# Performance work log

Measured on AMD Instinct MI355X. Metric: run time of the kernel, lower is better.

## Reference

```python
import jax, jax.numpy as jnp
import numpy as np

D_MODEL = 1024
NUM_HEADS = 16
DEPTH = D_MODEL // NUM_HEADS


def setup_inputs() -> dict:
    key = jax.random.key(0)
    ks = jax.random.split(key, 11)
    B, S, D = 2, 2048, D_MODEL
    s = 1.0 / np.sqrt(D)
    inp = {
        'x': jax.random.normal(ks[0], (B, S, D), jnp.float32),
        'pH': jax.random.normal(ks[1], (B, 1, 1), jnp.float32),
        'Wq': jax.random.normal(ks[2], (D, D), jnp.float32) * s,
        'bq': jnp.zeros((D,), jnp.float32),
        'Wk': jax.random.normal(ks[3], (D, D), jnp.float32) * s,
        'bk': jnp.zeros((D,), jnp.float32),
        'Wv': jax.random.normal(ks[4], (D, D), jnp.float32) * s,
        'bv': jnp.zeros((D,), jnp.float32),
        'Wo': jax.random.normal(ks[5], (D, D), jnp.float32) * s,
        'bo': jnp.zeros((D,), jnp.float32),
    }
    return inp


def reference(x, pH, Wq, bq, Wk, bk, Wv, bv, Wo, bo):
    B, S, D = x.shape
    H, dh = NUM_HEADS, DEPTH
    # QKV projections -> [B, H, S, dh]
    def proj(W, b):
        return (x @ W + b).reshape(B, S, H, dh).transpose(0, 2, 1, 3)
    q = proj(Wq, bq)
    k = proj(Wk, bk)
    v = proj(Wv, bv)
    # scores [B, H, S, S] with additive per-sample pH bias broadcast over heads/positions
    scores = jnp.einsum('bhqd,bhkd->bhqk', q, k) / jnp.sqrt(jnp.asarray(dh, x.dtype))
    scores = scores + pH[:, :, :, None]  # [B,1,1,1] broadcasts to [B,H,S,S]
    attn = jax.nn.softmax(scores, axis=-1)
    out = jnp.einsum('bhqk,bhkd->bhqd', attn, v)  # [B,H,S,dh]
    out = out.transpose(0, 2, 1, 3).reshape(B, S, D)
    return out @ Wo + bo  # dropout p=0.0 -> identity
```

## Files before the change

### kernel.cpp

```cpp
#include <hip/hip_runtime.h>
#include <hip/hip_bf16.h>
#include <math.h>

#define BATCH 2
#define SEQ   2048
#define DMODEL 1024
#define NHEADS 16
#define DHEAD 64
#define MROWS (BATCH*SEQ)

typedef __attribute__((ext_vector_type(8))) short bf16x8;
typedef __attribute__((ext_vector_type(4))) short bf16x4;
typedef __attribute__((ext_vector_type(4))) float f32x4;

__device__ __forceinline__ short f2bf(float f) {
    union { float f; unsigned u; } c; c.f = f;
    unsigned r = (c.u + 0x7fffu + ((c.u >> 16) & 1u)) >> 16;
    return (short)r;
}
__device__ __forceinline__ float bf2f(short h) {
    union { unsigned u; float f; } c; c.u = ((unsigned)(unsigned short)h) << 16;
    return c.f;
}

__device__ __forceinline__ void async_ld16(const void* g, void* l) {
    __builtin_amdgcn_global_load_lds(
        (const __attribute__((address_space(1))) unsigned*)g,
        (__attribute__((address_space(3))) unsigned*)l, 16, 0, 0);
}

__device__ __forceinline__ void pl32swap(unsigned &a, unsigned &b) {
    asm("v_permlane32_swap_b32 %0, %1" : "+v"(a), "+v"(b));
}
__device__ __forceinline__ void pl16swap(unsigned &a, unsigned &b) {
    asm("v_permlane16_swap_b32 %0, %1" : "+v"(a), "+v"(b));
}
__device__ __forceinline__ bf16x8 mk8(unsigned a, unsigned b, unsigned c, unsigned d) {
    union { unsigned u[4]; bf16x8 h; } t;
    t.u[0] = a; t.u[1] = b; t.u[2] = c; t.u[3] = d; return t.h;
}

__global__ __launch_bounds__(256) void prep(
    const float* __restrict__ x, short* __restrict__ xhi,
    const float* __restrict__ W0, const float* __restrict__ W1,
    const float* __restrict__ W2, const float* __restrict__ W3,
    short* __restrict__ oqkv, short* __restrict__ oo)
{
    __shared__ float T[64][65];
    const int tid = threadIdx.x;
    if (blockIdx.x < 2048) {
        const int i = blockIdx.x * 256 + tid;
        const float4* p = (const float4*)x + (size_t)i * 2;
        float4 a = p[0], b = p[1];
        float v[8] = {a.x, a.y, a.z, a.w, b.x, b.y, b.z, b.w};
        bf16x8 H;
        #pragma unroll
        for (int j = 0; j < 8; ++j) H[j] = f2bf(v[j]);
        *((bf16x8*)xhi + i) = H;
        return;
    }
    const int bi = blockIdx.x - 2048;
    const int z = bi >> 8;
    const int t = bi & 255;
    const float* W = (z == 0) ? W0 : (z == 1) ? W1 : (z == 2) ? W2 : W3;
    short* out = (z < 3) ? (oqkv + (size_t)z * 1024 * 1024) : oo;
    const int n0 = (t & 15) * 64, k0 = (t >> 4) * 64;
    #pragma unroll
    for (int i = 0; i < 16; ++i) {
        const int idx = tid + i * 256;
        const int r = idx >> 6, c = idx & 63;
        T[r][c] = W[(size_t)(k0 + r) * DMODEL + n0 + c];
    }
    __syncthreads();
    #pragma unroll
    for (int i = 0; i < 4; ++i) {
        const int idx = tid + i * 256;
        const int r = idx >> 4, g = idx & 15;
        bf16x4 H;
        #pragma unroll
        for (int j = 0; j < 4; ++j)
            H[j] = f2bf(T[g * 4 + j][r]);
        *(bf16x4*)(out + (size_t)(n0 + r) * DMODEL + k0 + g * 4) = H;
    }
}

__global__ __launch_bounds__(256, 3) void qkv_gemm(
    const short* __restrict__ Ahi, const short* __restrict__ Bthi,
    const float* __restrict__ b0, const float* __restrict__ b1, const float* __restrict__ b2,
    short* __restrict__ oqh, short* __restrict__ okh, short* __restrict__ ovh,
    float qscale)
{
    __shared__ short Ah[128 * 64], Bh[128 * 64];

    const int tid  = threadIdx.x;
    const int lane = tid & 63;
    const int w    = tid >> 6;
    const int quad = lane >> 4;
    const int l15  = lane & 15;
    const int wr   = w >> 1, wc = w & 1;
    const int m0   = blockIdx.y * 128;
    const int n0   = blockIdx.x * 128;
    const int K    = DMODEL;

    f32x4 acc[4][4] = {};

    for (int k0 = 0; k0 < K; k0 += 64) {
        __syncthreads();
        #pragma unroll
        for (int j = 0; j < 8; ++j) {
            const int base = w * 512 + j * 64;
            const int c = base + lane;
            if (base < 1024) {
                const int row = c >> 3, pos = (c & 7) ^ (row & 7);
                async_ld16(Ahi + (size_t)(m0 + row) * K + k0 + pos * 8, Ah + base * 8);
            } else {
                const int cb = c - 1024;
                const int row = cb >> 3, pos = (cb & 7) ^ (row & 7);
                async_ld16(Bthi + (size_t)(n0 + row) * K + k0 + pos * 8, Bh + (base - 1024) * 8);
            }
        }
        __syncthreads();

        #pragma unroll
        for (int s = 0; s < 2; ++s) {
            bf16x8 afh[4], bfh[4];
            #pragma unroll
            for (int mi = 0; mi < 4; ++mi) {
                const int row = wr * 64 + mi * 16 + l15;
                const int pos = (s * 4 + quad) ^ (row & 7);
                afh[mi] = *(const bf16x8*)(Ah + row * 64 + pos * 8);
            }
            #pragma unroll
            for (int ni = 0; ni < 4; ++ni) {
                const int row = wc * 64 + ni * 16 + l15;
                const int pos = (s * 4 + quad) ^ (row & 7);
                bfh[ni] = *(const bf16x8*)(Bh + row * 64 + pos * 8);
            }
            #pragma unroll
            for (int mi = 0; mi < 4; ++mi)
                #pragma unroll
                for (int ni = 0; ni < 4; ++ni)
                    acc[mi][ni] = __builtin_amdgcn_mfma_f32_16x16x32_bf16(
                        afh[mi], bfh[ni], acc[mi][ni], 0, 0, 0);
        }
    }

    const int nbase = n0 + wc * 64;
    const int which = nbase >> 10;
    const int hh = (nbase & 1023) >> 6;
    const int mb = m0 + wr * 64;
    const int b = mb >> 11, sbase = mb & (SEQ - 1);
    __syncthreads();
    short* scr = (w < 2) ? (Ah + w * 4096) : (Bh + (w - 2) * 4096);

    if (which < 2) {
        const float* bias = which ? b1 : b0;
        short* dstp = which ? okh : oqh;
        const float scl = which ? 1.0f : qscale;
        #pragma unroll
        for (int mi = 0; mi < 4; ++mi)
            #pragma unroll
            for (int ni = 0; ni < 4; ++ni)
                #pragma unroll
                for (int r = 0; r < 4; ++r) {
                    const int sloc = mi * 16 + quad * 4 + r;
                    const int dloc = ni * 16 + l15;
                    const int nn = (nbase + ni * 16 + l15) & 1023;
                    scr[sloc * 64 + (((dloc >> 3) ^ (sloc & 7)) * 8) + (dloc & 7)] =
                        f2bf((acc[mi][ni][r] + bias[nn]) * scl);
                }
        #pragma unroll
        for (int i = 0; i < 8; ++i) {
            const int sloc = i * 8 + (lane >> 3);
            const int cph = (lane & 7) ^ (sloc & 7);
            bf16x8 row = *(const bf16x8*)(scr + sloc * 64 + cph * 8);
            const int dloc = (lane & 7) * 8;
            *(bf16x8*)(dstp + ((size_t)(b * NHEADS + hh) * SEQ + sbase + sloc) * DHEAD + dloc) = row;
        }
    } else {
        #pragma unroll
        for (int mi = 0; mi < 4; ++mi)
            #pragma unroll
            for (int ni = 0; ni < 4; ++ni)
                #pragma unroll
                for (int r = 0; r < 4; ++r) {
                    const int sloc = mi * 16 + quad * 4 + r;
                    const int dloc = ni * 16 + l15;
                    const int nn = (nbase + ni * 16 + l15) & 1023;
                    scr[dloc * 64 + (((sloc >> 3) ^ (dloc & 7)) * 8) + (sloc & 7)] =
                        f2bf(acc[mi][ni][r] + b2[nn]);
                }
        #pragma unroll
        for (int i = 0; i < 8; ++i) {
            const int dloc = i * 8 + (lane >> 3);
            const int cph = (lane & 7) ^ (dloc & 7);
            bf16x8 row = *(const bf16x8*)(scr + dloc * 64 + cph * 8);
            const int sg = sbase + (lane & 7) * 8;
            *(bf16x8*)(ovh + ((size_t)(b * NHEADS + hh) * DHEAD + dloc) * SEQ + sg) = row;
        }
    }
}

__global__ __launch_bounds__(256) void ogemm(
    const short* __restrict__ Ahi, const short* __restrict__ Bthi,
    const float* __restrict__ b0, float* __restrict__ outf)
{
    __shared__ short Ah[64 * 64], Bh[128 * 64];

    const int tid  = threadIdx.x;
    const int lane = tid & 63;
    const int w    = tid >> 6;
    const int quad = lane >> 4;
    const int l15  = lane & 15;
    const int wr   = w >> 1, wc = w & 1;
    const int m0   = blockIdx.y * 64;
    const int n0   = blockIdx.x * 128;
    const int K    = DMODEL;

    f32x4 acc[2][4] = {};

    for (int k0 = 0; k0 < K; k0 += 64) {
        __syncthreads();
        #pragma unroll
        for (int j = 0; j < 6; ++j) {
            const int base = w * 384 + j * 64;
            const int c = base + lane;
            if (base < 512) {
                const int row = c >> 3, pos = (c & 7) ^ (row & 7);
                async_ld16(Ahi + (size_t)(m0 + row) * K + k0 + pos * 8, Ah + base * 8);
            } else {
                const int cb = c - 512;
                const int row = cb >> 3, pos = (cb & 7) ^ (row & 7);
                async_ld16(Bthi + (size_t)(n0 + row) * K + k0 + pos * 8, Bh + (base - 512) * 8);
            }
        }
        __syncthreads();

        #pragma unroll
        for (int s = 0; s < 2; ++s) {
            bf16x8 afh[2], bfh[4];
            #pragma unroll
            for (int mi = 0; mi < 2; ++mi) {
                const int row = wr * 32 + mi * 16 + l15;
                const int pos = (s * 4 + quad) ^ (row & 7);
                afh[mi] = *(const bf16x8*)(Ah + row * 64 + pos * 8);
            }
            #pragma unroll
            for (int ni = 0; ni < 4; ++ni) {
                const int row = wc * 64 + ni * 16 + l15;
                const int pos = (s * 4 + quad) ^ (row & 7);
                bfh[ni] = *(const bf16x8*)(Bh + row * 64 + pos * 8);
            }
            #pragma unroll
            for (int mi = 0; mi < 2; ++mi)
                #pragma unroll
                for (int ni = 0; ni < 4; ++ni)
                    acc[mi][ni] = __builtin_amdgcn_mfma_f32_16x16x32_bf16(
                        afh[mi], bfh[ni], acc[mi][ni], 0, 0, 0);
        }
    }

    #pragma unroll
    for (int mi = 0; mi < 2; ++mi)
        #pragma unroll
        for (int ni = 0; ni < 4; ++ni)
            #pragma unroll
            for (int r = 0; r < 4; ++r) {
                const int m = m0 + wr * 32 + mi * 16 + quad * 4 + r;
                const int nn = n0 + wc * 64 + ni * 16 + l15;
                outf[(size_t)m * DMODEL + nn] = acc[mi][ni][r] + b0[nn];
            }
}

__global__ __launch_bounds__(256) void attn_mfma(
    const short* __restrict__ Qh_g, const short* __restrict__ Kh_g,
    const short* __restrict__ Vth_g,
    short* __restrict__ op0, float* __restrict__ l0g)
{
    __shared__ short Ksh[4096];
    __shared__ short Vsh[4096];

    const int tid  = threadIdx.x;
    const int lane = tid & 63;
    const int w    = tid >> 6;
    const int quad = lane >> 4;
    const int l15  = lane & 15;

    const int bh    = blockIdx.x & 31;
    const int sk    = (blockIdx.x >> 5) & 3;
    const int qtile = blockIdx.x >> 7;
    const int q0    = qtile * 128 + w * 32;
    const size_t kvb = (size_t)bh * SEQ * DHEAD;

    bf16x8 ones;
    #pragma unroll
    for (int j = 0; j < 8; ++j) ones[j] = (short)0x3f80;

    bf16x8 qA[2], qB[2];
    {
        const size_t qrA = kvb + (size_t)(q0 + l15) * DHEAD;
        const size_t qrB = kvb + (size_t)(q0 + 16 + l15) * DHEAD;
        qA[0] = *(const bf16x8*)(Qh_g + qrA + quad * 8);
        qA[1] = *(const bf16x8*)(Qh_g + qrA + 32 + quad * 8);
        qB[0] = *(const bf16x8*)(Qh_g + qrB + quad * 8);
        qB[1] = *(const bf16x8*)(Qh_g + qrB + 32 + quad * 8);
    }

    const bool isv = (w >= 2);
    short* dst = isv ? Vsh : Ksh;
    int goff[4]; short* ldst[4];
    #pragma unroll
    for (int j = 0; j < 4; ++j) {
        const int c = (w & 1) * 256 + j * 64 + lane;
        const int row = c >> 3, pos = (c & 7) ^ (row & 7);
        goff[j] = isv ? (row * SEQ + pos * 8) : (row * DHEAD + pos * 8);
        ldst[j] = dst + (size_t)c * 8;
    }

    const int kb0 = sk * (SEQ / 4), kb1 = kb0 + SEQ / 4;
    const int step = isv ? 64 : 64 * DHEAD;
    const short* src = isv ? (Vth_g + kvb + kb0) : (Kh_g + kvb + (size_t)kb0 * DHEAD);

    f32x4 oA[4] = {}, oB[4] = {};
    f32x4 lAv = {}, lBv = {};

    bf16x8 stg[4];
    #pragma unroll
    for (int j = 0; j < 4; ++j) stg[j] = *(const bf16x8*)(src + goff[j]);
    src += step;

    for (int kb = kb0; kb < kb1; kb += 64) {
        __syncthreads();
        #pragma unroll
        for (int j = 0; j < 4; ++j) *(bf16x8*)ldst[j] = stg[j];
        __syncthreads();
        if (kb + 64 < kb1) {
            #pragma unroll
            for (int j = 0; j < 4; ++j) stg[j] = *(const bf16x8*)(src + goff[j]);
            src += step;
        }

        unsigned pa[8], pb[8];
        #pragma unroll
        for (int mf = 0; mf < 4; ++mf) {
            const int row = mf * 16 + l15;
            const int sw = row & 7;
            bf16x8 kh0 = *(const bf16x8*)(Ksh + row * 64 + ((quad ^ sw) * 8));
            bf16x8 kh1 = *(const bf16x8*)(Ksh + row * 64 + (((4 + quad) ^ sw) * 8));
            f32x4 cA = {}, cB = {};
            cA = __builtin_amdgcn_mfma_f32_16x16x32_bf16(kh0, qA[0], cA, 0, 0, 0);
            cA = __builtin_amdgcn_mfma_f32_16x16x32_bf16(kh1, qA[1], cA, 0, 0, 0);
            cB = __builtin_amdgcn_mfma_f32_16x16x32_bf16(kh0, qB[0], cB, 0, 0, 0);
            cB = __builtin_amdgcn_mfma_f32_16x16x32_bf16(kh1, qB[1], cB, 0, 0, 0);

            unsigned uA[4], uB[4];
            #pragma unroll
            for (int r = 0; r < 4; ++r) {
                union { float f; unsigned u; } p;
                p.f = __builtin_amdgcn_exp2f(cA[r]);
                uA[r] = p.u;
                p.f = __builtin_amdgcn_exp2f(cB[r]);
                uB[r] = p.u;
            }
            pa[mf * 2]     = __builtin_amdgcn_perm(uA[1], uA[0], 0x07060302u);
            pa[mf * 2 + 1] = __builtin_amdgcn_perm(uA[3], uA[2], 0x07060302u);
            pb[mf * 2]     = __builtin_amdgcn_perm(uB[1], uB[0], 0x07060302u);
            pb[mf * 2 + 1] = __builtin_amdgcn_perm(uB[3], uB[2], 0x07060302u);
        }

        pl32swap(pa[0], pa[2]); pl32swap(pa[1], pa[3]);
        pl32swap(pa[4], pa[6]); pl32swap(pa[5], pa[7]);
        pl16swap(pa[0], pa[2]); pl16swap(pa[1], pa[3]);
        pl16swap(pa[4], pa[6]); pl16swap(pa[5], pa[7]);
        pl32swap(pb[0], pb[2]); pl32swap(pb[1], pb[3]);
        pl32swap(pb[4], pb[6]); pl32swap(pb[5], pb[7]);
        pl16swap(pb[0], pb[2]); pl16swap(pb[1], pb[3]);
        pl16swap(pb[4], pb[6]); pl16swap(pb[5], pb[7]);
        bf16x8 pA0 = mk8(pa[0], pa[1], pa[2], pa[3]);
        bf16x8 pA1 = mk8(pa[4], pa[5], pa[6], pa[7]);
        bf16x8 pB0 = mk8(pb[0], pb[1], pb[2], pb[3]);
        bf16x8 pB1 = mk8(pb[4], pb[5], pb[6], pb[7]);

        lAv = __builtin_amdgcn_mfma_f32_16x16x32_bf16(pA0, ones, lAv, 0, 0, 0);
        lAv = __builtin_amdgcn_mfma_f32_16x16x32_bf16(pA1, ones, lAv, 0, 0, 0);
        lBv = __builtin_amdgcn_mfma_f32_16x16x32_bf16(pB0, ones, lBv, 0, 0, 0);
        lBv = __builtin_amdgcn_mfma_f32_16x16x32_bf16(pB1, ones, lBv, 0, 0, 0);

        #pragma unroll
        for (int nf = 0; nf < 4; ++nf) {
            const int row = nf * 16 + l15;
            const int sw = row & 7;
            bf16x8 vh0 = *(const bf16x8*)(Vsh + row * 64 + ((quad ^ sw) * 8));
            bf16x8 vh1 = *(const bf16x8*)(Vsh + row * 64 + (((4 + quad) ^ sw) * 8));
            f32x4 cA = oA[nf], cB = oB[nf];
            cA = __builtin_amdgcn_mfma_f32_16x16x32_bf16(pA0, vh0, cA, 0, 0, 0);
            cA = __builtin_amdgcn_mfma_f32_16x16x32_bf16(pA1, vh1, cA, 0, 0, 0);
            cB = __builtin_amdgcn_mfma_f32_16x16x32_bf16(pB0, vh0, cB, 0, 0, 0);
            cB = __builtin_amdgcn_mfma_f32_16x16x32_bf16(pB1, vh1, cB, 0, 0, 0);
            oA[nf] = cA;
            oB[nf] = cB;
        }
    }

    short* op = op0 + (size_t)sk * 4194304;
    float* lg = l0g + sk * 65536;
    const int b = bh >> 4, hh = bh & 15;
    #pragma unroll
    for (int r = 0; r < 4; ++r) {
        const int qa = q0 + quad * 4 + r;
        if (l15 == 0) {
            lg[bh * SEQ + qa] = lAv[r];
            lg[bh * SEQ + qa + 16] = lBv[r];
        }
    }
    #pragma unroll
    for (int nf = 0; nf < 4; ++nf) {
        #pragma unroll
        for (int r = 0; r < 4; ++r) {
            const int qa = q0 + quad * 4 + r;
            const int d = nf * 16 + l15;
            op[(size_t)(b * SEQ + qa) * DMODEL + hh * DHEAD + d] = f2bf(oA[nf][r]);
            op[(size_t)(b * SEQ + qa + 16) * DMODEL + hh * DHEAD + d] = f2bf(oB[nf][r]);
        }
    }
}

__global__ __launch_bounds__(256) void combine_o(
    const short* __restrict__ op0, const float* __restrict__ l0g,
    short* __restrict__ aoh)
{
    const int i = blockIdx.x * 256 + threadIdx.x;
    const size_t e = (size_t)i * 8;
    const int qg = (int)(e >> 10);
    const int col = (int)(e & 1023);
    const int b = qg >> 11;
    const int q = qg & (SEQ - 1);
    const int bhq = (b * NHEADS + (col >> 6)) * SEQ + q;
    const float inv = 1.0f / (l0g[bhq] + l0g[bhq + 65536] +
                              l0g[bhq + 2 * 65536] + l0g[bhq + 3 * 65536]);

    bf16x8 a0 = *((const bf16x8*)op0 + i);
    bf16x8 a1 = *((const bf16x8*)(op0 + 4194304) + i);
    bf16x8 a2 = *((const bf16x8*)(op0 + 2 * 4194304) + i);
    bf16x8 a3 = *((const bf16x8*)(op0 + 3 * 4194304) + i);
    bf16x8 H;
    #pragma unroll
    for (int j = 0; j < 8; ++j)
        H[j] = f2bf((bf2f(a0[j]) + bf2f(a1[j]) + bf2f(a2[j]) + bf2f(a3[j])) * inv);
    *((bf16x8*)aoh + i) = H;
}

extern "C" void kernel_launch(void* const* d_in, const int* in_sizes, int n_in,
                              void* d_out, int out_size, void* d_ws, size_t ws_size,
                              hipStream_t stream) {
    const float* x  = (const float*)d_in[0];
    const float* Wq = (const float*)d_in[2];
    const float* bq = (const float*)d_in[3];
    const float* Wk = (const float*)d_in[4];
    const float* bk = (const float*)d_in[5];
    const float* Wv = (const float*)d_in[6];
    const float* bv = (const float*)d_in[7];
    const float* Wo = (const float*)d_in[8];
    const float* bo = (const float*)d_in[9];
    float* out = (float*)d_out;

    char* ws = (char*)d_ws;
    const size_t MB = 1024 * 1024;
    short* qh  = (short*)(ws + 0 * MB);
    short* kh  = (short*)(ws + 16 * MB);
    short* vth = (short*)(ws + 32 * MB);
    short* aoh = (short*)(ws + 48 * MB);
    short* op0 = (short*)(ws + 56 * MB);
    short* xhi = (short*)(ws + 64 * MB);
    short* wqkv_hi = (short*)(ws + 80 * MB);
    float* l0g = (float*)(ws + 88 * MB);
    short* wto_hi  = (short*)(ws + 92 * MB);

    dim3 blk(256);

    hipLaunchKernelGGL(prep, dim3(2048 + 1024), blk, 0, stream,
                       x, xhi, Wq, Wk, Wv, Wo, wqkv_hi, wto_hi);

    const float qscale = 0.125f * 1.44269504088896f;
    hipLaunchKernelGGL(qkv_gemm, dim3(3072 / 128, MROWS / 128), blk, 0, stream,
                       xhi, wqkv_hi, bq, bk, bv, qh, kh, vth, qscale);

    hipLaunchKernelGGL(attn_mfma, dim3(BATCH * NHEADS * (SEQ / 128) * 4), blk, 0, stream,
                       qh, kh, vth, op0, l0g);

    hipLaunchKernelGGL(combine_o, dim3(MROWS * DMODEL / 8 / 256), blk, 0, stream,
                       op0, l0g, aoh);

    hipLaunchKernelGGL(ogemm, dim3(1024 / 128, MROWS / 64), blk, 0, stream,
                       aoh, wto_hi, bo, out);
}
```

Baseline: 193.4 us.

## Load K and V fragments directly from global memory instead of LDS staging

```diff
diff --git a/kernel.cpp b/kernel.cpp
--- a/kernel.cpp
+++ b/kernel.cpp
@@ -277,9 +277,6 @@
     const short* __restrict__ Vth_g,
     short* __restrict__ op0, float* __restrict__ l0g)
 {
-    __shared__ short Ksh[4096];
-    __shared__ short Vsh[4096];
-
     const int tid  = threadIdx.x;
     const int lane = tid & 63;
     const int w    = tid >> 6;
@@ -306,47 +303,21 @@
         qB[1] = *(const bf16x8*)(Qh_g + qrB + 32 + quad * 8);
     }
 
-    const bool isv = (w >= 2);
-    short* dst = isv ? Vsh : Ksh;
-    int goff[4]; short* ldst[4];
-    #pragma unroll
-    for (int j = 0; j < 4; ++j) {
-        const int c = (w & 1) * 256 + j * 64 + lane;
-        const int row = c >> 3, pos = (c & 7) ^ (row & 7);
-        goff[j] = isv ? (row * SEQ + pos * 8) : (row * DHEAD + pos * 8);
-        ldst[j] = dst + (size_t)c * 8;
-    }
+    const short* Kp = Kh_g + kvb + (size_t)l15 * DHEAD + quad * 8;
+    const short* Vp = Vth_g + kvb + (size_t)l15 * SEQ + quad * 8;
 
     const int kb0 = sk * (SEQ / 4), kb1 = kb0 + SEQ / 4;
-    const int step = isv ? 64 : 64 * DHEAD;
-    const short* src = isv ? (Vth_g + kvb + kb0) : (Kh_g + kvb + (size_t)kb0 * DHEAD);
 
     f32x4 oA[4] = {}, oB[4] = {};
     f32x4 lAv = {}, lBv = {};
 
-    bf16x8 stg[4];
-    #pragma unroll
-    for (int j = 0; j < 4; ++j) stg[j] = *(const bf16x8*)(src + goff[j]);
-    src += step;
-
     for (int kb = kb0; kb < kb1; kb += 64) {
-        __syncthreads();
-        #pragma unroll
-        for (int j = 0; j < 4; ++j) *(bf16x8*)ldst[j] = stg[j];
-        __syncthreads();
-        if (kb + 64 < kb1) {
-            #pragma unroll
-            for (int j = 0; j < 4; ++j) stg[j] = *(const bf16x8*)(src + goff[j]);
-            src += step;
-        }
-
         unsigned pa[8], pb[8];
         #pragma unroll
         for (int mf = 0; mf < 4; ++mf) {
-            const int row = mf * 16 + l15;
-            const int sw = row & 7;
-            bf16x8 kh0 = *(const bf16x8*)(Ksh + row * 64 + ((quad ^ sw) * 8));
-            bf16x8 kh1 = *(const bf16x8*)(Ksh + row * 64 + (((4 + quad) ^ sw) * 8));
+            const short* kr = Kp + (size_t)(kb + mf * 16) * DHEAD;
+            bf16x8 kh0 = *(const bf16x8*)(kr);
+            bf16x8 kh1 = *(const bf16x8*)(kr + 32);
             f32x4 cA = {}, cB = {};
             cA = __builtin_amdgcn_mfma_f32_16x16x32_bf16(kh0, qA[0], cA, 0, 0, 0);
             cA = __builtin_amdgcn_mfma_f32_16x16x32_bf16(kh1, qA[1], cA, 0, 0, 0);
@@ -388,10 +359,9 @@
 
         #pragma unroll
         for (int nf = 0; nf < 4; ++nf) {
-            const int row = nf * 16 + l15;
-            const int sw = row & 7;
-            bf16x8 vh0 = *(const bf16x8*)(Vsh + row * 64 + ((quad ^ sw) * 8));
-            bf16x8 vh1 = *(const bf16x8*)(Vsh + row * 64 + (((4 + quad) ^ sw) * 8));
+            const short* vr = Vp + (size_t)(nf * 16) * SEQ + kb;
+            bf16x8 vh0 = *(const bf16x8*)(vr);
+            bf16x8 vh1 = *(const bf16x8*)(vr + 32);
             f32x4 cA = oA[nf], cB = oB[nf];
             cA = __builtin_amdgcn_mfma_f32_16x16x32_bf16(pA0, vh0, cA, 0, 0, 0);
             cA = __builtin_amdgcn_mfma_f32_16x16x32_bf16(pA1, vh1, cA, 0, 0, 0);
```

After: 267.8 us. +38.5%, slower.
